# Optimization experiments

Hardware: AMD Instinct MI355X
Metric: run time of the kernel (lower is better)

Reference implementation:

```python
import jax, jax.numpy as jnp
import numpy as np

N_NODES = 50000
N_EDGES = 800000
IN_CH = 16
OUT_CH = 16


def setup_inputs() -> dict:
    key = jax.random.key(0)
    ks = jax.random.split(key, 12)
    s = lambda d: 1.0 / np.sqrt(d)
    return {
        "x": jax.random.normal(ks[0], (N_NODES, IN_CH), jnp.float32),
        "edge_index": jax.random.randint(ks[1], (2, N_EDGES), 0, N_NODES, jnp.int64),
        "edge_attr": jax.random.uniform(ks[2], (N_EDGES, 8), jnp.float32),
        "W1": jax.random.normal(ks[3], (8, 100), jnp.float32) * s(8),
        "b1": jnp.zeros((100,), jnp.float32),
        "W2": jax.random.normal(ks[4], (100, 100), jnp.float32) * s(100),
        "b2": jnp.zeros((100,), jnp.float32),
        "W3": jax.random.normal(ks[5], (100, 100), jnp.float32) * s(100),
        "b3": jnp.zeros((100,), jnp.float32),
        "W4": jax.random.normal(ks[6], (100, IN_CH * OUT_CH), jnp.float32) * s(100),
        "b4": jnp.zeros((IN_CH * OUT_CH,), jnp.float32),
        "root": jax.random.normal(ks[7], (IN_CH, OUT_CH), jnp.float32) * s(IN_CH),
        "bias": jnp.zeros((OUT_CH,), jnp.float32),
    }


def reference(x, edge_index, edge_attr, W1, b1, W2, b2, W3, b3, W4, b4, root, bias):
    src, dst = edge_index[0], edge_index[1]
    # edge MLP -> per-edge weight matrix [E, in, out]
    h = jax.nn.relu(edge_attr @ W1 + b1)
    h = jax.nn.relu(h @ W2 + b2)
    h = jax.nn.relu(h @ W3 + b3)
    w = (h @ W4 + b4).reshape(-1, IN_CH, OUT_CH)
    # gather source features, per-edge matmul
    msg = jnp.einsum('ei,eio->eo', x[src], w)  # [E, out]
    # scatter-mean into destination nodes
    agg = jax.ops.segment_sum(msg, dst, num_segments=N_NODES)
    cnt = jax.ops.segment_sum(jnp.ones((msg.shape[0],), msg.dtype), dst, num_segments=N_NODES)
    agg = agg / jnp.maximum(cnt, 1.0)[:, None]
    return x @ root + agg + bias
```

## Files before the change

kernel.cpp:

```cpp
#include <hip/hip_runtime.h>
#include <hip/hip_bf16.h>

constexpr int N_NODES = 50000;
constexpr int E_TOTAL = 800000;
constexpr int EB   = 128;
constexpr int NT   = E_TOTAL / EB;
constexpr int GRID = 256;
constexpr int TPB  = 512;

typedef __attribute__((ext_vector_type(8)))  short bf16x8;
typedef __attribute__((ext_vector_type(16))) float f32x16;

constexpr size_t WS_CNT = 0;
constexpr size_t WS_W1  = 200704;
constexpr size_t WS_W2  = WS_W1 + 4096;
constexpr size_t WS_W3  = WS_W2 + 32768;
constexpr size_t WS_W4  = WS_W3 + 32768;

constexpr int L_HA  = 0;
constexpr int L_HB  = 34816;
constexpr int L_EA  = 69632;
constexpr int L_XS  = 75776;
constexpr int L_MSG = 86016;
constexpr int L_DST = 126976;
constexpr int L_TOT = 128000;

__device__ inline unsigned short bfb(float f) {
    __hip_bfloat16 h = __float2bfloat16(f);
    return __builtin_bit_cast(unsigned short, h);
}
__device__ inline unsigned pk2(float a, float b) {
    return (unsigned)bfb(a) | ((unsigned)bfb(b) << 16);
}
__device__ inline unsigned pk2r(float a, float b) {
    return pk2(fmaxf(a, 0.f), fmaxf(b, 0.f));
}

template<int IN_OFF, int OUT_OFF>
__device__ inline void layer32(char* sm, const bf16x8 (&wf)[8],
                               int wn, int we, int l31, int g)
{
    f32x16 acc[2] = {};
#pragma unroll
    for (int ks = 0; ks < 8; ++ks) {
        bf16x8 b[2];
#pragma unroll
        for (int ef = 0; ef < 2; ++ef) {
            const int e = 64 * we + 32 * ef + l31;
            b[ef] = *reinterpret_cast<const bf16x8*>(sm + IN_OFF + e * 272 + ks * 32 + g * 16);
        }
#pragma unroll
        for (int ef = 0; ef < 2; ++ef)
            acc[ef] = __builtin_amdgcn_mfma_f32_32x32x16_bf16(wf[ks], b[ef], acc[ef], 0, 0, 0);
    }
#pragma unroll
    for (int ef = 0; ef < 2; ++ef) {
        const int e = 64 * we + 32 * ef + l31;
#pragma unroll
        for (int q = 0; q < 4; ++q) {
            uint2 pk;
            pk.x = pk2r(acc[ef][4 * q + 0], acc[ef][4 * q + 1]);
            pk.y = pk2r(acc[ef][4 * q + 2], acc[ef][4 * q + 3]);
            *reinterpret_cast<uint2*>(sm + OUT_OFF + e * 272 + 64 * wn + 16 * q + 8 * g) = pk;
        }
    }
}

__global__ __launch_bounds__(TPB, 2)
void edge_kernel(const float* __restrict__ x, const int* __restrict__ eidx,
                 const float* __restrict__ ea, const char* __restrict__ ws,
                 float* __restrict__ out, float* __restrict__ cnt)
{
    extern __shared__ char sm[];
    const int t    = threadIdx.x;
    const int lane = t & 63;
    const int wave = t >> 6;
    const int wn   = wave & 3, we = wave >> 2;
    const int l31  = lane & 31, g = lane >> 5;
    int* dsti = reinterpret_cast<int*>(sm + L_DST);

    bf16x8 wf1, wf2[8], wf3[8], wf4[2][8];
    {
        const int n = 32 * wn + l31;
        wf1 = *reinterpret_cast<const bf16x8*>(ws + WS_W1 + n * 32 + g * 16);
#pragma unroll
        for (int ks = 0; ks < 8; ++ks) {
            wf2[ks] = *reinterpret_cast<const bf16x8*>(ws + WS_W2 + n * 256 + ks * 32 + g * 16);
            wf3[ks] = *reinterpret_cast<const bf16x8*>(ws + WS_W3 + n * 256 + ks * 32 + g * 16);
        }
#pragma unroll
        for (int mf = 0; mf < 2; ++mf) {
            const int n4 = 64 * wn + 32 * mf + l31;
#pragma unroll
            for (int ks = 0; ks < 8; ++ks)
                wf4[mf][ks] = *reinterpret_cast<const bf16x8*>(ws + WS_W4 + n4 * 256 + ks * 32 + g * 16);
        }
    }

    if (t < 128)
        *reinterpret_cast<uint4*>(sm + L_EA + t * 48 + 16) = make_uint4(0x3F80u, 0u, 0u, 0u);

    float4 eaR, xvR; int dstR = 0;
    {
        const int e0 = blockIdx.x * EB;
        if (t < 256) eaR = *reinterpret_cast<const float4*>(&ea[(size_t)(e0 + (t >> 1)) * 8 + (t & 1) * 4]);
        const int s = eidx[e0 + (t >> 2)];
        xvR = *reinterpret_cast<const float4*>(&x[(size_t)s * 16 + (t & 3) * 4]);
        if (t < 128) dstR = eidx[E_TOTAL + e0 + t];
    }

    int p = 0;
    bool has_prev = false;
    for (int tile = blockIdx.x; tile < NT; tile += GRID) {
        if (has_prev) {
            const int e = t >> 2, o0 = (t & 3) * 4;
            float4 s0 = *reinterpret_cast<const float4*>(sm + L_MSG + 0 * 10240 + e * 80 + o0 * 4);
            const float4 s1 = *reinterpret_cast<const float4*>(sm + L_MSG + 1 * 10240 + e * 80 + o0 * 4);
            const float4 s2 = *reinterpret_cast<const float4*>(sm + L_MSG + 2 * 10240 + e * 80 + o0 * 4);
            const float4 s3 = *reinterpret_cast<const float4*>(sm + L_MSG + 3 * 10240 + e * 80 + o0 * 4);
            const int d = dsti[(p ^ 1) * 128 + e];
            unsafeAtomicAdd(&out[(size_t)d * 16 + o0 + 0], s0.x + s1.x + s2.x + s3.x);
            unsafeAtomicAdd(&out[(size_t)d * 16 + o0 + 1], s0.y + s1.y + s2.y + s3.y);
            unsafeAtomicAdd(&out[(size_t)d * 16 + o0 + 2], s0.z + s1.z + s2.z + s3.z);
            unsafeAtomicAdd(&out[(size_t)d * 16 + o0 + 3], s0.w + s1.w + s2.w + s3.w);
            if ((t & 3) == 0) unsafeAtomicAdd(&cnt[d], 1.0f);
        }
        if (t < 256) {
            uint2 pk; pk.x = pk2(eaR.x, eaR.y); pk.y = pk2(eaR.z, eaR.w);
            *reinterpret_cast<uint2*>(sm + L_EA + (t >> 1) * 48 + 8 * (t & 1)) = pk;
        }
        *reinterpret_cast<float4*>(sm + L_XS + (t >> 2) * 80 + (t & 3) * 16) = xvR;
        if (t < 128) dsti[p * 128 + t] = dstR;

        const int nxt = tile + GRID;
        if (nxt < NT) {
            const int e0 = nxt * EB;
            if (t < 256) eaR = *reinterpret_cast<const float4*>(&ea[(size_t)(e0 + (t >> 1)) * 8 + (t & 1) * 4]);
            const int s = eidx[e0 + (t >> 2)];
            xvR = *reinterpret_cast<const float4*>(&x[(size_t)s * 16 + (t & 3) * 4]);
            if (t < 128) dstR = eidx[E_TOTAL + e0 + t];
        }
        __syncthreads();

        {
            f32x16 acc[2] = {};
#pragma unroll
            for (int ef = 0; ef < 2; ++ef) {
                const int e = 64 * we + 32 * ef + l31;
                const bf16x8 b = *reinterpret_cast<const bf16x8*>(sm + L_EA + e * 48 + g * 16);
                acc[ef] = __builtin_amdgcn_mfma_f32_32x32x16_bf16(wf1, b, acc[ef], 0, 0, 0);
            }
#pragma unroll
            for (int ef = 0; ef < 2; ++ef) {
                const int e = 64 * we + 32 * ef + l31;
#pragma unroll
                for (int q = 0; q < 4; ++q) {
                    uint2 pk;
                    pk.x = pk2r(acc[ef][4 * q + 0], acc[ef][4 * q + 1]);
                    pk.y = pk2r(acc[ef][4 * q + 2], acc[ef][4 * q + 3]);
                    *reinterpret_cast<uint2*>(sm + L_HA + e * 272 + 64 * wn + 16 * q + 8 * g) = pk;
                }
            }
        }
        __syncthreads();
        layer32<L_HA, L_HB>(sm, wf2, wn, we, l31, g);
        __syncthreads();
        layer32<L_HB, L_HA>(sm, wf3, wn, we, l31, g);
        __syncthreads();

        {
            f32x16 acc4[2][2] = {};
#pragma unroll
            for (int ks = 0; ks < 8; ++ks) {
                bf16x8 b[2];
#pragma unroll
                for (int ef = 0; ef < 2; ++ef) {
                    const int e = 64 * we + 32 * ef + l31;
                    b[ef] = *reinterpret_cast<const bf16x8*>(sm + L_HA + e * 272 + ks * 32 + g * 16);
                }
#pragma unroll
                for (int mf = 0; mf < 2; ++mf)
#pragma unroll
                    for (int ef = 0; ef < 2; ++ef)
                        acc4[mf][ef] = __builtin_amdgcn_mfma_f32_32x32x16_bf16(wf4[mf][ks], b[ef], acc4[mf][ef], 0, 0, 0);
            }
#pragma unroll
            for (int ef = 0; ef < 2; ++ef) {
                const int e = 64 * we + 32 * ef + l31;
                const float4 xv = *reinterpret_cast<const float4*>(sm + L_XS + e * 80 + wn * 16);
                float pr[8] = {0.f, 0.f, 0.f, 0.f, 0.f, 0.f, 0.f, 0.f};
#pragma unroll
                for (int mf = 0; mf < 2; ++mf)
#pragma unroll
                    for (int reg = 0; reg < 16; ++reg) {
                        const float xi = (&xv.x)[2 * mf + (reg >> 3)];
                        const int s = (reg & 3) + 4 * ((reg >> 2) & 1);
                        pr[s] = fmaf(xi, acc4[mf][ef][reg], pr[s]);
                    }
                *reinterpret_cast<float4*>(sm + L_MSG + wn * 10240 + e * 80 + 16 * g) =
                    make_float4(pr[0], pr[1], pr[2], pr[3]);
                *reinterpret_cast<float4*>(sm + L_MSG + wn * 10240 + e * 80 + 32 + 16 * g) =
                    make_float4(pr[4], pr[5], pr[6], pr[7]);
            }
        }
        __syncthreads();
        p ^= 1;
        has_prev = true;
    }

    if (has_prev) {
        const int e = t >> 2, o0 = (t & 3) * 4;
        const float4 s0 = *reinterpret_cast<const float4*>(sm + L_MSG + 0 * 10240 + e * 80 + o0 * 4);
        const float4 s1 = *reinterpret_cast<const float4*>(sm + L_MSG + 1 * 10240 + e * 80 + o0 * 4);
        const float4 s2 = *reinterpret_cast<const float4*>(sm + L_MSG + 2 * 10240 + e * 80 + o0 * 4);
        const float4 s3 = *reinterpret_cast<const float4*>(sm + L_MSG + 3 * 10240 + e * 80 + o0 * 4);
        const int d = dsti[(p ^ 1) * 128 + e];
        unsafeAtomicAdd(&out[(size_t)d * 16 + o0 + 0], s0.x + s1.x + s2.x + s3.x);
        unsafeAtomicAdd(&out[(size_t)d * 16 + o0 + 1], s0.y + s1.y + s2.y + s3.y);
        unsafeAtomicAdd(&out[(size_t)d * 16 + o0 + 2], s0.z + s1.z + s2.z + s3.z);
        unsafeAtomicAdd(&out[(size_t)d * 16 + o0 + 3], s0.w + s1.w + s2.w + s3.w);
        if ((t & 3) == 0) unsafeAtomicAdd(&cnt[d], 1.0f);
    }
}

__global__ __launch_bounds__(256)
void prep_kernel(const float* __restrict__ W1, const float* __restrict__ b1,
                 const float* __restrict__ W2, const float* __restrict__ b2,
                 const float* __restrict__ W3, const float* __restrict__ b3,
                 const float* __restrict__ W4, const float* __restrict__ b4,
                 char* __restrict__ ws)
{
    const int id = blockIdx.x * 256 + threadIdx.x;
    if (id < N_NODES) reinterpret_cast<float*>(ws + WS_CNT)[id] = 0.f;
    if (id >= 67584) return;
    if (id < 2048) {
        const int n = id >> 4, k = id & 15;
        float v = 0.f;
        if (k < 8)        { if (n < 100) v = W1[k * 100 + n]; }
        else if (k == 8)  { v = (n < 100) ? b1[n] : (n == 100 ? 1.f : 0.f); }
        reinterpret_cast<unsigned short*>(ws + WS_W1)[id] = bfb(v);
    } else if (id < 18432) {
        const int j = id - 2048, n = j >> 7, k = j & 127;
        float v = 0.f;
        if (k < 100)       { if (n < 100) v = W2[k * 100 + n]; }
        else if (k == 100) { v = (n < 100) ? b2[n] : (n == 100 ? 1.f : 0.f); }
        reinterpret_cast<unsigned short*>(ws + WS_W2)[j] = bfb(v);
    } else if (id < 34816) {
        const int j = id - 18432, n = j >> 7, k = j & 127;
        float v = 0.f;
        if (k < 100)       { if (n < 100) v = W3[k * 100 + n]; }
        else if (k == 100) { v = (n < 100) ? b3[n] : (n == 100 ? 1.f : 0.f); }
        reinterpret_cast<unsigned short*>(ws + WS_W3)[j] = bfb(v);
    } else {
        const int j = id - 34816, n = j >> 7, k = j & 127;
        float v = 0.f;
        if (k < 100)       v = W4[k * 256 + n];
        else if (k == 100) v = b4[n];
        reinterpret_cast<unsigned short*>(ws + WS_W4)[j] = bfb(v);
    }
}

__global__ __launch_bounds__(256)
void node_kernel(const float* __restrict__ x, const float* __restrict__ root,
                 const float* __restrict__ bias, const float* __restrict__ cnt,
                 float* __restrict__ out)
{
    const int n = blockIdx.x * blockDim.x + threadIdx.x;
    if (n >= N_NODES) return;
    float xr[16];
#pragma unroll
    for (int q = 0; q < 4; ++q) {
        const float4 v = *reinterpret_cast<const float4*>(&x[(size_t)n * 16 + 4 * q]);
        xr[4 * q] = v.x; xr[4 * q + 1] = v.y; xr[4 * q + 2] = v.z; xr[4 * q + 3] = v.w;
    }
    const float inv = 1.f / fmaxf(cnt[n], 1.f);
#pragma unroll
    for (int q = 0; q < 4; ++q) {
        float4 o4 = *reinterpret_cast<float4*>(&out[(size_t)n * 16 + 4 * q]);
        float res[4];
#pragma unroll
        for (int j = 0; j < 4; ++j) {
            const int o = 4 * q + j;
            float dot = 0.f;
#pragma unroll
            for (int i = 0; i < 16; ++i)
                dot = fmaf(xr[i], root[i * 16 + o], dot);
            res[j] = dot + (&o4.x)[j] * inv + bias[o];
        }
        *reinterpret_cast<float4*>(&out[(size_t)n * 16 + 4 * q]) = make_float4(res[0], res[1], res[2], res[3]);
    }
}

extern "C" void kernel_launch(void* const* d_in, const int* in_sizes, int n_in,
                              void* d_out, int out_size, void* d_ws, size_t ws_size,
                              hipStream_t stream)
{
    const float* x    = (const float*)d_in[0];
    const int*   eidx = (const int*)  d_in[1];
    const float* ea   = (const float*)d_in[2];
    const float* W1   = (const float*)d_in[3];
    const float* b1   = (const float*)d_in[4];
    const float* W2   = (const float*)d_in[5];
    const float* b2   = (const float*)d_in[6];
    const float* W3   = (const float*)d_in[7];
    const float* b3   = (const float*)d_in[8];
    const float* W4   = (const float*)d_in[9];
    const float* b4   = (const float*)d_in[10];
    const float* root = (const float*)d_in[11];
    const float* bias = (const float*)d_in[12];
    float* out = (float*)d_out;
    char*  ws  = (char*)d_ws;
    float* cnt = (float*)d_ws;

    (void)in_sizes; (void)n_in; (void)ws_size;

    hipFuncSetAttribute((const void*)edge_kernel,
                        hipFuncAttributeMaxDynamicSharedMemorySize, L_TOT);

    hipMemsetAsync(d_out, 0, (size_t)out_size * sizeof(float), stream);

    hipLaunchKernelGGL(prep_kernel, dim3(264), dim3(256), 0, stream,
                       W1, b1, W2, b2, W3, b3, W4, b4, ws);
    hipLaunchKernelGGL(edge_kernel, dim3(GRID), dim3(TPB), L_TOT, stream,
                       x, eidx, ea, ws, out, cnt);
    hipLaunchKernelGGL(node_kernel, dim3((N_NODES + 255) / 256), dim3(256), 0, stream,
                       x, root, bias, cnt, out);
}
```

Measured before the change: 328.8 us.

## Halve edge tile to 64 and raise occupancy to four blocks per CU

Shrinks the per-block edge tile from 128 to 64 edges, doubles the persistent grid, and lets each wave handle one 32-edge MFMA fragment instead of two. Shared memory per block is halved and launch bounds now ask for four blocks per CU, so the barrier-heavy layer pipeline has more resident waves to hide latency. In exchange each wave does less MFMA work between barriers, and only half the threads take part in the gather and atomic scatter phases. The lower accumulator count may also cut register pressure enough to reach that occupancy.

```diff
diff --git a/kernel.cpp b/kernel.cpp
--- a/kernel.cpp
+++ b/kernel.cpp
@@ -3,9 +3,9 @@
 
 constexpr int N_NODES = 50000;
 constexpr int E_TOTAL = 800000;
-constexpr int EB   = 128;
+constexpr int EB   = 64;
 constexpr int NT   = E_TOTAL / EB;
-constexpr int GRID = 256;
+constexpr int GRID = 512;
 constexpr int TPB  = 512;
 
 typedef __attribute__((ext_vector_type(8)))  short bf16x8;
@@ -18,12 +18,12 @@
 constexpr size_t WS_W4  = WS_W3 + 32768;
 
 constexpr int L_HA  = 0;
-constexpr int L_HB  = 34816;
-constexpr int L_EA  = 69632;
-constexpr int L_XS  = 75776;
-constexpr int L_MSG = 86016;
-constexpr int L_DST = 126976;
-constexpr int L_TOT = 128000;
+constexpr int L_HB  = 17408;
+constexpr int L_EA  = 34816;
+constexpr int L_XS  = 37888;
+constexpr int L_MSG = 43008;
+constexpr int L_DST = 63488;
+constexpr int L_TOT = 64000;
 
 __device__ inline unsigned short bfb(float f) {
     __hip_bfloat16 h = __float2bfloat16(f);
@@ -40,33 +40,23 @@
 __device__ inline void layer32(char* sm, const bf16x8 (&wf)[8],
                                int wn, int we, int l31, int g)
 {
-    f32x16 acc[2] = {};
+    const int e = 32 * we + l31;
+    f32x16 acc = {};
 #pragma unroll
     for (int ks = 0; ks < 8; ++ks) {
-        bf16x8 b[2];
-#pragma unroll
-        for (int ef = 0; ef < 2; ++ef) {
-            const int e = 64 * we + 32 * ef + l31;
-            b[ef] = *reinterpret_cast<const bf16x8*>(sm + IN_OFF + e * 272 + ks * 32 + g * 16);
-        }
-#pragma unroll
-        for (int ef = 0; ef < 2; ++ef)
-            acc[ef] = __builtin_amdgcn_mfma_f32_32x32x16_bf16(wf[ks], b[ef], acc[ef], 0, 0, 0);
-    }
-#pragma unroll
-    for (int ef = 0; ef < 2; ++ef) {
-        const int e = 64 * we + 32 * ef + l31;
-#pragma unroll
-        for (int q = 0; q < 4; ++q) {
-            uint2 pk;
-            pk.x = pk2r(acc[ef][4 * q + 0], acc[ef][4 * q + 1]);
-            pk.y = pk2r(acc[ef][4 * q + 2], acc[ef][4 * q + 3]);
-            *reinterpret_cast<uint2*>(sm + OUT_OFF + e * 272 + 64 * wn + 16 * q + 8 * g) = pk;
-        }
-    }
-}
-
-__global__ __launch_bounds__(TPB, 2)
+        const bf16x8 b = *reinterpret_cast<const bf16x8*>(sm + IN_OFF + e * 272 + ks * 32 + g * 16);
+        acc = __builtin_amdgcn_mfma_f32_32x32x16_bf16(wf[ks], b, acc, 0, 0, 0);
+    }
+#pragma unroll
+    for (int q = 0; q < 4; ++q) {
+        uint2 pk;
+        pk.x = pk2r(acc[4 * q + 0], acc[4 * q + 1]);
+        pk.y = pk2r(acc[4 * q + 2], acc[4 * q + 3]);
+        *reinterpret_cast<uint2*>(sm + OUT_OFF + e * 272 + 64 * wn + 16 * q + 8 * g) = pk;
+    }
+}
+
+__global__ __launch_bounds__(TPB, 4)
 void edge_kernel(const float* __restrict__ x, const int* __restrict__ eidx,
                  const float* __restrict__ ea, const char* __restrict__ ws,
                  float* __restrict__ out, float* __restrict__ cnt)
@@ -97,124 +87,112 @@
         }
     }
 
-    if (t < 128)
+    if (t < 64)
         *reinterpret_cast<uint4*>(sm + L_EA + t * 48 + 16) = make_uint4(0x3F80u, 0u, 0u, 0u);
 
     float4 eaR, xvR; int dstR = 0;
     {
         const int e0 = blockIdx.x * EB;
-        if (t < 256) eaR = *reinterpret_cast<const float4*>(&ea[(size_t)(e0 + (t >> 1)) * 8 + (t & 1) * 4]);
-        const int s = eidx[e0 + (t >> 2)];
-        xvR = *reinterpret_cast<const float4*>(&x[(size_t)s * 16 + (t & 3) * 4]);
-        if (t < 128) dstR = eidx[E_TOTAL + e0 + t];
+        if (t < 128) eaR = *reinterpret_cast<const float4*>(&ea[(size_t)(e0 + (t >> 1)) * 8 + (t & 1) * 4]);
+        if (t < 256) {
+            const int s = eidx[e0 + (t >> 2)];
+            xvR = *reinterpret_cast<const float4*>(&x[(size_t)s * 16 + (t & 3) * 4]);
+        }
+        if (t < 64) dstR = eidx[E_TOTAL + e0 + t];
     }
 
     int p = 0;
     bool has_prev = false;
     for (int tile = blockIdx.x; tile < NT; tile += GRID) {
-        if (has_prev) {
+        if (has_prev && t < 256) {
             const int e = t >> 2, o0 = (t & 3) * 4;
-            float4 s0 = *reinterpret_cast<const float4*>(sm + L_MSG + 0 * 10240 + e * 80 + o0 * 4);
-            const float4 s1 = *reinterpret_cast<const float4*>(sm + L_MSG + 1 * 10240 + e * 80 + o0 * 4);
-            const float4 s2 = *reinterpret_cast<const float4*>(sm + L_MSG + 2 * 10240 + e * 80 + o0 * 4);
-            const float4 s3 = *reinterpret_cast<const float4*>(sm + L_MSG + 3 * 10240 + e * 80 + o0 * 4);
-            const int d = dsti[(p ^ 1) * 128 + e];
+            const float4 s0 = *reinterpret_cast<const float4*>(sm + L_MSG + 0 * 5120 + e * 80 + o0 * 4);
+            const float4 s1 = *reinterpret_cast<const float4*>(sm + L_MSG + 1 * 5120 + e * 80 + o0 * 4);
+            const float4 s2 = *reinterpret_cast<const float4*>(sm + L_MSG + 2 * 5120 + e * 80 + o0 * 4);
+            const float4 s3 = *reinterpret_cast<const float4*>(sm + L_MSG + 3 * 5120 + e * 80 + o0 * 4);
+            const int d = dsti[(p ^ 1) * 64 + e];
             unsafeAtomicAdd(&out[(size_t)d * 16 + o0 + 0], s0.x + s1.x + s2.x + s3.x);
             unsafeAtomicAdd(&out[(size_t)d * 16 + o0 + 1], s0.y + s1.y + s2.y + s3.y);
             unsafeAtomicAdd(&out[(size_t)d * 16 + o0 + 2], s0.z + s1.z + s2.z + s3.z);
             unsafeAtomicAdd(&out[(size_t)d * 16 + o0 + 3], s0.w + s1.w + s2.w + s3.w);
             if ((t & 3) == 0) unsafeAtomicAdd(&cnt[d], 1.0f);
         }
-        if (t < 256) {
+        if (t < 128) {
             uint2 pk; pk.x = pk2(eaR.x, eaR.y); pk.y = pk2(eaR.z, eaR.w);
             *reinterpret_cast<uint2*>(sm + L_EA + (t >> 1) * 48 + 8 * (t & 1)) = pk;
         }
-        *reinterpret_cast<float4*>(sm + L_XS + (t >> 2) * 80 + (t & 3) * 16) = xvR;
-        if (t < 128) dsti[p * 128 + t] = dstR;
+        if (t < 256)
+            *reinterpret_cast<float4*>(sm + L_XS + (t >> 2) * 80 + (t & 3) * 16) = xvR;
+        if (t < 64) dsti[p * 64 + t] = dstR;
 
         const int nxt = tile + GRID;
         if (nxt < NT) {
             const int e0 = nxt * EB;
-            if (t < 256) eaR = *reinterpret_cast<const float4*>(&ea[(size_t)(e0 + (t >> 1)) * 8 + (t & 1) * 4]);
-            const int s = eidx[e0 + (t >> 2)];
-            xvR = *reinterpret_cast<const float4*>(&x[(size_t)s * 16 + (t & 3) * 4]);
-            if (t < 128) dstR = eidx[E_TOTAL + e0 + t];
+            if (t < 128) eaR = *reinterpret_cast<const float4*>(&ea[(size_t)(e0 + (t >> 1)) * 8 + (t & 1) * 4]);
+            if (t < 256) {
+                const int s = eidx[e0 + (t >> 2)];
+                xvR = *reinterpret_cast<const float4*>(&x[(size_t)s * 16 + (t & 3) * 4]);
+            }
+            if (t < 64) dstR = eidx[E_TOTAL + e0 + t];
         }
         __syncthreads();
 
         {
-            f32x16 acc[2] = {};
-#pragma unroll
-            for (int ef = 0; ef < 2; ++ef) {
-                const int e = 64 * we + 32 * ef + l31;
-                const bf16x8 b = *reinterpret_cast<const bf16x8*>(sm + L_EA + e * 48 + g * 16);
-                acc[ef] = __builtin_amdgcn_mfma_f32_32x32x16_bf16(wf1, b, acc[ef], 0, 0, 0);
+            const int e = 32 * we + l31;
+            const bf16x8 b = *reinterpret_cast<const bf16x8*>(sm + L_EA + e * 48 + g * 16);
+            f32x16 acc = {};
+            acc = __builtin_amdgcn_mfma_f32_32x32x16_bf16(wf1, b, acc, 0, 0, 0);
+#pragma unroll
+            for (int q = 0; q < 4; ++q) {
+                uint2 pk;
+                pk.x = pk2r(acc[4 * q + 0], acc[4 * q + 1]);
+                pk.y = pk2r(acc[4 * q + 2], acc[4 * q + 3]);
+                *reinterpret_cast<uint2*>(sm + L_HA + e * 272 + 64 * wn + 16 * q + 8 * g) = pk;
             }
-#pragma unroll
-            for (int ef = 0; ef < 2; ++ef) {
-                const int e = 64 * we + 32 * ef + l31;
-#pragma unroll
-                for (int q = 0; q < 4; ++q) {
-                    uint2 pk;
-                    pk.x = pk2r(acc[ef][4 * q + 0], acc[ef][4 * q + 1]);
-                    pk.y = pk2r(acc[ef][4 * q + 2], acc[ef][4 * q + 3]);
-                    *reinterpret_cast<uint2*>(sm + L_HA + e * 272 + 64 * wn + 16 * q + 8 * g) = pk;
+        }
+        __syncthreads();
+        layer32<L_HA, L_HB>(sm, wf2, wn, we, l31, g);
+        __syncthreads();
+        layer32<L_HB, L_HA>(sm, wf3, wn, we, l31, g);
+        __syncthreads();
+
+        {
+            const int e = 32 * we + l31;
+            f32x16 acc4[2] = {};
+#pragma unroll
+            for (int ks = 0; ks < 8; ++ks) {
+                const bf16x8 b = *reinterpret_cast<const bf16x8*>(sm + L_HA + e * 272 + ks * 32 + g * 16);
+#pragma unroll
+                for (int mf = 0; mf < 2; ++mf)
+                    acc4[mf] = __builtin_amdgcn_mfma_f32_32x32x16_bf16(wf4[mf][ks], b, acc4[mf], 0, 0, 0);
+            }
+            const float4 xv = *reinterpret_cast<const float4*>(sm + L_XS + e * 80 + wn * 16);
+            float pr[8] = {0.f, 0.f, 0.f, 0.f, 0.f, 0.f, 0.f, 0.f};
+#pragma unroll
+            for (int mf = 0; mf < 2; ++mf)
+#pragma unroll
+                for (int reg = 0; reg < 16; ++reg) {
+                    const float xi = (&xv.x)[2 * mf + (reg >> 3)];
+                    const int s = (reg & 3) + 4 * ((reg >> 2) & 1);
+                    pr[s] = fmaf(xi, acc4[mf][reg], pr[s]);
                 }
-            }
-        }
-        __syncthreads();
-        layer32<L_HA, L_HB>(sm, wf2, wn, we, l31, g);
-        __syncthreads();
-        layer32<L_HB, L_HA>(sm, wf3, wn, we, l31, g);
-        __syncthreads();
-
-        {
-            f32x16 acc4[2][2] = {};
-#pragma unroll
-            for (int ks = 0; ks < 8; ++ks) {
-                bf16x8 b[2];
-#pragma unroll
-                for (int ef = 0; ef < 2; ++ef) {
-                    const int e = 64 * we + 32 * ef + l31;
-                    b[ef] = *reinterpret_cast<const bf16x8*>(sm + L_HA + e * 272 + ks * 32 + g * 16);
-                }
-#pragma unroll
-                for (int mf = 0; mf < 2; ++mf)
-#pragma unroll
-                    for (int ef = 0; ef < 2; ++ef)
-                        acc4[mf][ef] = __builtin_amdgcn_mfma_f32_32x32x16_bf16(wf4[mf][ks], b[ef], acc4[mf][ef], 0, 0, 0);
-            }
-#pragma unroll
-            for (int ef = 0; ef < 2; ++ef) {
-                const int e = 64 * we + 32 * ef + l31;
-                const float4 xv = *reinterpret_cast<const float4*>(sm + L_XS + e * 80 + wn * 16);
-                float pr[8] = {0.f, 0.f, 0.f, 0.f, 0.f, 0.f, 0.f, 0.f};
-#pragma unroll
-                for (int mf = 0; mf < 2; ++mf)
-#pragma unroll
-                    for (int reg = 0; reg < 16; ++reg) {
-                        const float xi = (&xv.x)[2 * mf + (reg >> 3)];
-                        const int s = (reg & 3) + 4 * ((reg >> 2) & 1);
-                        pr[s] = fmaf(xi, acc4[mf][ef][reg], pr[s]);
-                    }
-                *reinterpret_cast<float4*>(sm + L_MSG + wn * 10240 + e * 80 + 16 * g) =
-                    make_float4(pr[0], pr[1], pr[2], pr[3]);
-                *reinterpret_cast<float4*>(sm + L_MSG + wn * 10240 + e * 80 + 32 + 16 * g) =
-                    make_float4(pr[4], pr[5], pr[6], pr[7]);
-            }
+            *reinterpret_cast<float4*>(sm + L_MSG + wn * 5120 + e * 80 + 16 * g) =
+                make_float4(pr[0], pr[1], pr[2], pr[3]);
+            *reinterpret_cast<float4*>(sm + L_MSG + wn * 5120 + e * 80 + 32 + 16 * g) =
+                make_float4(pr[4], pr[5], pr[6], pr[7]);
         }
         __syncthreads();
         p ^= 1;
         has_prev = true;
     }
 
-    if (has_prev) {
+    if (has_prev && t < 256) {
         const int e = t >> 2, o0 = (t & 3) * 4;
-        const float4 s0 = *reinterpret_cast<const float4*>(sm + L_MSG + 0 * 10240 + e * 80 + o0 * 4);
-        const float4 s1 = *reinterpret_cast<const float4*>(sm + L_MSG + 1 * 10240 + e * 80 + o0 * 4);
-        const float4 s2 = *reinterpret_cast<const float4*>(sm + L_MSG + 2 * 10240 + e * 80 + o0 * 4);
-        const float4 s3 = *reinterpret_cast<const float4*>(sm + L_MSG + 3 * 10240 + e * 80 + o0 * 4);
-        const int d = dsti[(p ^ 1) * 128 + e];
+        const float4 s0 = *reinterpret_cast<const float4*>(sm + L_MSG + 0 * 5120 + e * 80 + o0 * 4);
+        const float4 s1 = *reinterpret_cast<const float4*>(sm + L_MSG + 1 * 5120 + e * 80 + o0 * 4);
+        const float4 s2 = *reinterpret_cast<const float4*>(sm + L_MSG + 2 * 5120 + e * 80 + o0 * 4);
+        const float4 s3 = *reinterpret_cast<const float4*>(sm + L_MSG + 3 * 5120 + e * 80 + o0 * 4);
+        const int d = dsti[(p ^ 1) * 64 + e];
         unsafeAtomicAdd(&out[(size_t)d * 16 + o0 + 0], s0.x + s1.x + s2.x + s3.x);
         unsafeAtomicAdd(&out[(size_t)d * 16 + o0 + 1], s0.y + s1.y + s2.y + s3.y);
         unsafeAtomicAdd(&out[(size_t)d * 16 + o0 + 2], s0.z + s1.z + s2.z + s3.z);
```

Result: slower. 450.8 us (+37.1%).
